# Performance work log

Hardware: AMD Instinct MI355X
Metric: run time of the kernel (lower is better)

## Reference

```python
import jax, jax.numpy as jnp
import numpy as np

N_VOX = 500_000
C = 128
HID = 4 * C
RES = 128  # voxel grid resolution
K_OFFS = 27


def _build_sparse_coords_and_neighbors(seed=0):
    rng = np.random.default_rng(seed)
    lin = rng.choice(RES ** 3, size=N_VOX, replace=False)
    z = lin // (RES * RES)
    y = (lin // RES) % RES
    x = lin % RES
    # padded grid (RES+2)^3 so boundary lookups are in-bounds
    P = RES + 2
    grid = -np.ones(P * P * P, dtype=np.int64)
    z1, y1, x1 = z + 1, y + 1, x + 1
    grid[z1 * P * P + y1 * P + x1] = np.arange(N_VOX)
    offs = np.array([[dz, dy, dx] for dz in (-1, 0, 1) for dy in (-1, 0, 1) for dx in (-1, 0, 1)], dtype=np.int64)  # [27,3]
    nz = z1[:, None] + offs[None, :, 0]
    ny = y1[:, None] + offs[None, :, 1]
    nx = x1[:, None] + offs[None, :, 2]
    nbr = grid[nz * P * P + ny * P + nx]  # [N,27], -1 if neighbor voxel inactive
    return nbr.astype(np.int32)


def setup_inputs() -> dict:
    key = jax.random.key(0)
    ks = jax.random.split(key, 8)
    nbr = _build_sparse_coords_and_neighbors()
    scale = 0.02
    return {
        "feats": jax.random.normal(ks[0], (N_VOX, C), jnp.float32),
        "neighbor_idx": jnp.asarray(nbr),
        "conv_w": jax.random.normal(ks[1], (K_OFFS, C, C), jnp.float32) * scale,
        "conv_b": jax.random.normal(ks[2], (C,), jnp.float32) * scale,
        "ln_g": jnp.ones((C,), jnp.float32),
        "ln_b": jnp.zeros((C,), jnp.float32),
        "w1": jax.random.normal(ks[3], (C, HID), jnp.float32) * scale,
        "b1": jax.random.normal(ks[4], (HID,), jnp.float32) * scale,
        "w2": jax.random.normal(ks[5], (HID, C), jnp.float32) * scale,
        "b2": jax.random.normal(ks[6], (C,), jnp.float32) * scale,
    }


def _forward(feats, neighbor_idx, conv_w, conv_b, ln_g, ln_b, w1, b1, w2, b2):
    n, c = feats.shape
    # submanifold sparse conv3d: pad a zero row for missing (-1) neighbors
    f_pad = jnp.concatenate([feats, jnp.zeros((1, c), feats.dtype)], axis=0)
    idx = jnp.where(neighbor_idx < 0, n, neighbor_idx)  # [N,27]
    h = jnp.broadcast_to(conv_b, (n, c))
    for k in range(K_OFFS):  # fixed small kernel-offset loop; per-offset gather + GEMM
        h = h + f_pad[idx[:, k]] @ conv_w[k]
    # LayerNorm32 (fp32 math), eps=1e-6, affine
    h32 = h.astype(jnp.float32)
    mu = h32.mean(-1, keepdims=True)
    var = h32.var(-1, keepdims=True)
    hn = ((h32 - mu) * jax.lax.rsqrt(var + 1e-6) * ln_g + ln_b).astype(feats.dtype)
    # MLP: Linear -> SiLU -> Linear
    m = jax.nn.silu(hn @ w1 + b1) @ w2 + b2
    # residual h + x on sparse feats
    return m + feats


def reference(feats, neighbor_idx, conv_w, conv_b, ln_g, ln_b, w1, b1, w2, b2):
    return _forward(feats, neighbor_idx, conv_w, conv_b, ln_g, ln_b, w1, b1, w2, b2)
```

## Files before the change

### kernel.cpp

```cpp
#include <hip/hip_runtime.h>
#include <stdint.h>

#define NVOX 500000
#define NPAD 500224
#define ZERO_OFF (NVOX * 128)

typedef float  f32x4  __attribute__((ext_vector_type(4)));
typedef short  short8 __attribute__((ext_vector_type(8)));

__device__ __forceinline__ short f2bf(float x){
  unsigned u = __float_as_uint(x);
  unsigned r = (u + 0x7fffu + ((u >> 16) & 1u)) >> 16;
  return (short)r;
}

__device__ __forceinline__ void gload_lds16(const void* g, void* l){
  __builtin_amdgcn_global_load_lds(
      (const __attribute__((address_space(1))) unsigned int*)(uintptr_t)g,
      (__attribute__((address_space(3))) unsigned int*)(unsigned int)(uintptr_t)l,
      16, 0, 0);
}

__global__ void cast_feats_kernel(const float* __restrict__ f, short* __restrict__ t){
  long i = ((long)blockIdx.x * 256 + threadIdx.x) * 8;
  float4 a = *(const float4*)(f + i);
  float4 b = *(const float4*)(f + i + 4);
  short8 o = { f2bf(a.x), f2bf(a.y), f2bf(a.z), f2bf(a.w),
               f2bf(b.x), f2bf(b.y), f2bf(b.z), f2bf(b.w) };
  *(short8*)(t + i) = o;
}

__global__ void prep_nbr_kernel(const int* __restrict__ nbr, int* __restrict__ nbrT){
  __shared__ int lds_n[6912];
  const int tid = threadIdx.x;
  const long base = (long)blockIdx.x * 6912;
  #pragma unroll
  for (int i = 0; i < 27; i++){
    long g = base + i*256 + tid;
    lds_n[i*256 + tid] = (g < (long)NVOX*27) ? nbr[g] : -1;
  }
  __syncthreads();
  const int row = blockIdx.x * 256 + tid;
  #pragma unroll
  for (int k = 0; k < 27; k++){
    int id = lds_n[tid*27 + k];
    nbrT[(size_t)k*NPAD + row] = (id < 0 ? NVOX : id) * 128;
  }
}

__global__ void prep_weights_kernel(const float* __restrict__ cw, const float* __restrict__ w1,
                                    const float* __restrict__ w2,
                                    short* __restrict__ cw_sw, short* __restrict__ w1_sw,
                                    short* __restrict__ w2_sw){
  int t = blockIdx.x * 256 + threadIdx.x;
  if (t < 55296){
    int k = t >> 11, rem = t & 2047;
    int nf = rem >> 8, ks = (rem >> 6) & 3, l = rem & 63;
    int g = l >> 4, c = l & 15;
    short8 o;
    #pragma unroll
    for (int j = 0; j < 8; j++){
      int kk = ks*32 + g*8 + j;
      o[j] = f2bf(cw[(k*128 + kk)*128 + nf*16 + c]);
    }
    *(short8*)(cw_sw + (size_t)t*8) = o;
  } else if (t < 63488){
    int u = t - 55296;
    int nf = u >> 8, ks = (u >> 6) & 3, l = u & 63;
    int g = l >> 4, c = l & 15;
    short8 o;
    #pragma unroll
    for (int j = 0; j < 8; j++){
      int kk = ks*32 + g*8 + j;
      o[j] = f2bf(w1[kk*512 + nf*16 + c]);
    }
    *(short8*)(w1_sw + (size_t)u*8) = o;
  } else {
    int u = t - 63488;
    int ch = u >> 10, rem = u & 1023;
    int nf = rem >> 7, ks2 = (rem >> 6) & 1, l = u & 63;
    int g = l >> 4, c = l & 15;
    short8 o;
    #pragma unroll
    for (int j = 0; j < 8; j++){
      int k = ch*64 + ks2*32 + g*8 + j;
      o[j] = f2bf(w2[k*128 + nf*16 + c]);
    }
    *(short8*)(w2_sw + (size_t)u*8) = o;
  }
}

__global__ __launch_bounds__(256, 2)
void conv_ln_pf_kernel(const short* __restrict__ table, const int* __restrict__ nbrT,
                       const short* __restrict__ cw_sw,
                       const float* __restrict__ conv_b, const float* __restrict__ ln_g,
                       const float* __restrict__ ln_b, short* __restrict__ hn16){
  __shared__ __align__(16) short lds_b[2][16384];
  const int tid = threadIdx.x;
  const int lane = tid & 63, wv = tid >> 6;
  const int l15 = lane & 15, lg = lane >> 4;
  const int rowbase = blockIdx.x * 256 + wv * 64;
  const int rowi = rowbase + l15;

  f32x4 acc[4][8];
  #pragma unroll
  for (int m = 0; m < 4; m++)
    #pragma unroll
    for (int n = 0; n < 8; n++)
      acc[m][n] = f32x4{0.f, 0.f, 0.f, 0.f};

  int idx_c[4], idx_n[4];
  #pragma unroll
  for (int m = 0; m < 4; m++) idx_c[m] = nbrT[rowi + m*16];
  #pragma unroll
  for (int m = 0; m < 4; m++) idx_n[m] = nbrT[NPAD + rowi + m*16];
  short8 afp[2][4];
  #pragma unroll
  for (int ks = 0; ks < 2; ks++)
    #pragma unroll
    for (int m = 0; m < 4; m++)
      afp[ks][m] = *(const short8*)(table + (size_t)(unsigned)idx_c[m] + ks*32 + lg*8);
  {
    const char* src = (const char*)cw_sw;
    char* dst = (char*)&lds_b[0][0];
    #pragma unroll
    for (int i = 0; i < 8; i++){ int off = i*4096 + tid*16; gload_lds16(src+off, dst+off); }
  }

  for (int k = 0; k < 27; k++){
    const int buf = k & 1;
    __syncthreads();
    short8 af2[4], af3[4];
    #pragma unroll
    for (int m = 0; m < 4; m++)
      af2[m] = *(const short8*)(table + (size_t)(unsigned)idx_c[m] + 64 + lg*8);
    #pragma unroll
    for (int m = 0; m < 4; m++)
      af3[m] = *(const short8*)(table + (size_t)(unsigned)idx_c[m] + 96 + lg*8);
    int idx_n2[4];
    #pragma unroll
    for (int m = 0; m < 4; m++)
      idx_n2[m] = (k + 2 < 27) ? nbrT[(size_t)(k+2)*NPAD + rowi + m*16] : ZERO_OFF;
    if (k + 1 < 27){
      const char* src = (const char*)cw_sw + (size_t)(k+1)*32768;
      char* dst = (char*)&lds_b[buf ^ 1][0];
      #pragma unroll
      for (int i = 0; i < 8; i++){ int off = i*4096 + tid*16; gload_lds16(src+off, dst+off); }
    }

    const short* bbase = &lds_b[buf][0];
    #pragma unroll
    for (int ks = 0; ks < 2; ks++){
      #pragma unroll
      for (int n = 0; n < 8; n++){
        short8 b = *(const short8*)(bbase + ((n*4 + ks)*64 + lane)*8);
        #pragma unroll
        for (int m = 0; m < 4; m++)
          acc[m][n] = __builtin_amdgcn_mfma_f32_16x16x32_bf16(afp[ks][m], b, acc[m][n], 0, 0, 0);
      }
    }
    short8 afp_n[2][4];
    #pragma unroll
    for (int ks = 0; ks < 2; ks++)
      #pragma unroll
      for (int m = 0; m < 4; m++)
        afp_n[ks][m] = *(const short8*)(table + (size_t)(unsigned)idx_n[m] + ks*32 + lg*8);
    #pragma unroll
    for (int n = 0; n < 8; n++){
      short8 b = *(const short8*)(bbase + ((n*4 + 2)*64 + lane)*8);
      #pragma unroll
      for (int m = 0; m < 4; m++)
        acc[m][n] = __builtin_amdgcn_mfma_f32_16x16x32_bf16(af2[m], b, acc[m][n], 0, 0, 0);
    }
    #pragma unroll
    for (int n = 0; n < 8; n++){
      short8 b = *(const short8*)(bbase + ((n*4 + 3)*64 + lane)*8);
      #pragma unroll
      for (int m = 0; m < 4; m++)
        acc[m][n] = __builtin_amdgcn_mfma_f32_16x16x32_bf16(af3[m], b, acc[m][n], 0, 0, 0);
    }
    #pragma unroll
    for (int m = 0; m < 4; m++){
      afp[0][m] = afp_n[0][m];
      afp[1][m] = afp_n[1][m];
      idx_c[m] = idx_n[m];
      idx_n[m] = idx_n2[m];
    }
  }

  float cb[8], g8[8], be[8];
  #pragma unroll
  for (int n = 0; n < 8; n++){
    cb[n] = conv_b[n*16 + l15];
    g8[n] = ln_g[n*16 + l15];
    be[n] = ln_b[n*16 + l15];
  }
  #pragma unroll
  for (int m = 0; m < 4; m++){
    #pragma unroll
    for (int r = 0; r < 4; r++){
      float s = 0.f, s2 = 0.f;
      #pragma unroll
      for (int n = 0; n < 8; n++){
        float h = acc[m][n][r] + cb[n];
        acc[m][n][r] = h;
        s += h; s2 += h*h;
      }
      #pragma unroll
      for (int msk = 1; msk < 16; msk <<= 1){
        s  += __shfl_xor(s,  msk);
        s2 += __shfl_xor(s2, msk);
      }
      float mu  = s  * 0.0078125f;
      float var = s2 * 0.0078125f - mu*mu;
      float rs  = rsqrtf(var + 1e-6f);
      int row = rowbase + m*16 + lg*4 + r;
      if (row < NVOX){
        #pragma unroll
        for (int n = 0; n < 8; n++){
          float hv = (acc[m][n][r] - mu) * rs * g8[n] + be[n];
          hn16[(size_t)row*128 + n*16 + l15] = f2bf(hv);
        }
      }
    }
  }
}

template<bool TBL>
__global__ __launch_bounds__(256, 2)
void conv_ln_kernel(const short* __restrict__ table, const float* __restrict__ feats,
                    const int* __restrict__ nbr, const short* __restrict__ cw_sw,
                    const float* __restrict__ conv_b, const float* __restrict__ ln_g,
                    const float* __restrict__ ln_b, short* __restrict__ hn16){
  __shared__ __align__(16) short lds_b[2][16384];
  const int tid = threadIdx.x;
  const int lane = tid & 63, wv = tid >> 6;
  const int l15 = lane & 15, lg = lane >> 4;
  const int rowbase = blockIdx.x * 256 + wv * 64;

  f32x4 acc[4][8];
  #pragma unroll
  for (int m = 0; m < 4; m++)
    #pragma unroll
    for (int n = 0; n < 8; n++)
      acc[m][n] = f32x4{0.f, 0.f, 0.f, 0.f};

  {
    const char* src = (const char*)cw_sw;
    char* dst = (char*)&lds_b[0][0];
    #pragma unroll
    for (int i = 0; i < 8; i++){ int off = i*4096 + tid*16; gload_lds16(src+off, dst+off); }
  }

  for (int k = 0; k < 27; k++){
    const int buf = k & 1;
    __syncthreads();
    if (k + 1 < 27){
      const char* src = (const char*)cw_sw + (size_t)(k+1)*32768;
      char* dst = (char*)&lds_b[buf ^ 1][0];
      #pragma unroll
      for (int i = 0; i < 8; i++){ int off = i*4096 + tid*16; gload_lds16(src+off, dst+off); }
    }
    int idxr[4];
    #pragma unroll
    for (int m = 0; m < 4; m++){
      int row = rowbase + m*16 + l15;
      row = row < NVOX ? row : NVOX - 1;
      int id = nbr[row*27 + k];
      idxr[m] = TBL ? (id < 0 ? NVOX : id) : id;
    }
    const short* bbase = &lds_b[buf][0];
    #pragma unroll
    for (int ks = 0; ks < 4; ks++){
      short8 af[4];
      #pragma unroll
      for (int m = 0; m < 4; m++){
        if constexpr (TBL){
          af[m] = *(const short8*)(table + (size_t)idxr[m]*128 + ks*32 + lg*8);
        } else {
          if (idxr[m] < 0){
            af[m] = short8{0,0,0,0,0,0,0,0};
          } else {
            const float* p = feats + (size_t)idxr[m]*128 + ks*32 + lg*8;
            float4 x = *(const float4*)p;
            float4 y = *(const float4*)(p + 4);
            af[m] = short8{ f2bf(x.x), f2bf(x.y), f2bf(x.z), f2bf(x.w),
                            f2bf(y.x), f2bf(y.y), f2bf(y.z), f2bf(y.w) };
          }
        }
      }
      #pragma unroll
      for (int n = 0; n < 8; n++){
        short8 b = *(const short8*)(bbase + ((n*4 + ks)*64 + lane)*8);
        #pragma unroll
        for (int m = 0; m < 4; m++)
          acc[m][n] = __builtin_amdgcn_mfma_f32_16x16x32_bf16(af[m], b, acc[m][n], 0, 0, 0);
      }
    }
  }

  float cb[8], g8[8], be[8];
  #pragma unroll
  for (int n = 0; n < 8; n++){
    cb[n] = conv_b[n*16 + l15];
    g8[n] = ln_g[n*16 + l15];
    be[n] = ln_b[n*16 + l15];
  }
  #pragma unroll
  for (int m = 0; m < 4; m++){
    #pragma unroll
    for (int r = 0; r < 4; r++){
      float s = 0.f, s2 = 0.f;
      #pragma unroll
      for (int n = 0; n < 8; n++){
        float h = acc[m][n][r] + cb[n];
        acc[m][n][r] = h;
        s += h; s2 += h*h;
      }
      #pragma unroll
      for (int msk = 1; msk < 16; msk <<= 1){
        s  += __shfl_xor(s,  msk);
        s2 += __shfl_xor(s2, msk);
      }
      float mu  = s  * 0.0078125f;
      float var = s2 * 0.0078125f - mu*mu;
      float rs  = rsqrtf(var + 1e-6f);
      int row = rowbase + m*16 + lg*4 + r;
      if (row < NVOX){
        #pragma unroll
        for (int n = 0; n < 8; n++){
          float hv = (acc[m][n][r] - mu) * rs * g8[n] + be[n];
          hn16[(size_t)row*128 + n*16 + l15] = f2bf(hv);
        }
      }
    }
  }
}

__global__ __launch_bounds__(256, 2)
void mlp_kernel(const short* __restrict__ hn16, const float* __restrict__ feats,
                const short* __restrict__ w1_sw, const short* __restrict__ w2_sw,
                const float* __restrict__ b1, const float* __restrict__ b2,
                float* __restrict__ out){
  __shared__ __align__(16) short lds_w[2][16384];
  __shared__ __align__(16) short lds_act[4*2048];
  const int tid = threadIdx.x;
  const int lane = tid & 63, wv = tid >> 6;
  const int l15 = lane & 15, lg = lane >> 4;
  const int rowbase = blockIdx.x * 128 + wv * 32;
  short* actw = &lds_act[wv * 2048];

  f32x4 acc2[2][8];
  #pragma unroll
  for (int m = 0; m < 2; m++)
    #pragma unroll
    for (int n = 0; n < 8; n++)
      acc2[m][n] = f32x4{0.f, 0.f, 0.f, 0.f};

  int rowg[2];
  #pragma unroll
  for (int m = 0; m < 2; m++){
    int row = rowbase + m*16 + l15;
    rowg[m] = row < NVOX ? row : NVOX - 1;
  }

  short8 a1[4][2];
  #pragma unroll
  for (int ks = 0; ks < 4; ks++)
    #pragma unroll
    for (int m = 0; m < 2; m++)
      a1[ks][m] = *(const short8*)(hn16 + (size_t)rowg[m]*128 + ks*32 + lg*8);

  {
    const char* s1 = (const char*)w1_sw;
    const char* s2 = (const char*)w2_sw;
    char* dst = (char*)&lds_w[0][0];
    #pragma unroll
    for (int i = 0; i < 4; i++){ int off = i*4096 + tid*16; gload_lds16(s1+off, dst+off); }
    #pragma unroll
    for (int i = 0; i < 4; i++){ int off = i*4096 + tid*16; gload_lds16(s2+off, dst+16384+off); }
  }

  for (int ch = 0; ch < 8; ch++){
    const int buf = ch & 1;
    __syncthreads();
    if (ch + 1 < 8){
      const char* s1 = (const char*)w1_sw + (size_t)(ch+1)*16384;
      const char* s2 = (const char*)w2_sw + (size_t)(ch+1)*16384;
      char* dst = (char*)&lds_w[buf ^ 1][0];
      #pragma unroll
      for (int i = 0; i < 4; i++){ int off = i*4096 + tid*16; gload_lds16(s1+off, dst+off); }
      #pragma unroll
      for (int i = 0; i < 4; i++){ int off = i*4096 + tid*16; gload_lds16(s2+off, dst+16384+off); }
    }
    const short* w1c = &lds_w[buf][0];
    const short* w2c = &lds_w[buf][8192];

    #pragma unroll
    for (int n = 0; n < 4; n++){
      f32x4 p0 = f32x4{0.f,0.f,0.f,0.f};
      f32x4 p1 = f32x4{0.f,0.f,0.f,0.f};
      #pragma unroll
      for (int ks = 0; ks < 4; ks++){
        short8 b = *(const short8*)(w1c + ((n*4 + ks)*64 + lane)*8);
        p0 = __builtin_amdgcn_mfma_f32_16x16x32_bf16(a1[ks][0], b, p0, 0, 0, 0);
        p1 = __builtin_amdgcn_mfma_f32_16x16x32_bf16(a1[ks][1], b, p1, 0, 0, 0);
      }
      float bb1 = b1[ch*64 + n*16 + l15];
      #pragma unroll
      for (int r = 0; r < 4; r++){
        float x0 = p0[r] + bb1;
        float x1 = p1[r] + bb1;
        float s0 = x0 / (1.f + __expf(-x0));
        float s1 = x1 / (1.f + __expf(-x1));
        int r0 = lg*4 + r;
        int r1 = 16 + lg*4 + r;
        actw[(r0*64 + n*16 + l15) ^ ((r0 & 7) << 3)] = f2bf(s0);
        actw[(r1*64 + n*16 + l15) ^ ((r1 & 7) << 3)] = f2bf(s1);
      }
    }

    #pragma unroll
    for (int ks2 = 0; ks2 < 2; ks2++){
      short8 a2[2];
      #pragma unroll
      for (int m = 0; m < 2; m++){
        int rowloc = m*16 + l15;
        a2[m] = *(const short8*)(actw + ((rowloc*64 + ks2*32 + lg*8) ^ ((rowloc & 7) << 3)));
      }
      #pragma unroll
      for (int n = 0; n < 8; n++){
        short8 b = *(const short8*)(w2c + ((n*2 + ks2)*64 + lane)*8);
        #pragma unroll
        for (int m = 0; m < 2; m++)
          acc2[m][n] = __builtin_amdgcn_mfma_f32_16x16x32_bf16(a2[m], b, acc2[m][n], 0, 0, 0);
      }
    }
  }

  float bb2[8];
  #pragma unroll
  for (int n = 0; n < 8; n++) bb2[n] = b2[n*16 + l15];
  #pragma unroll
  for (int m = 0; m < 2; m++)
    #pragma unroll
    for (int n = 0; n < 8; n++)
      #pragma unroll
      for (int r = 0; r < 4; r++){
        int row = rowbase + m*16 + lg*4 + r;
        if (row < NVOX){
          size_t ci = (size_t)row*128 + n*16 + l15;
          out[ci] = acc2[m][n][r] + bb2[n] + feats[ci];
        }
      }
}

extern "C" void kernel_launch(void* const* d_in, const int* in_sizes, int n_in,
                              void* d_out, int out_size, void* d_ws, size_t ws_size,
                              hipStream_t stream){
  const float* feats = (const float*)d_in[0];
  const int*   nbr   = (const int*)  d_in[1];
  const float* cw    = (const float*)d_in[2];
  const float* cb    = (const float*)d_in[3];
  const float* lng   = (const float*)d_in[4];
  const float* lnb   = (const float*)d_in[5];
  const float* w1    = (const float*)d_in[6];
  const float* b1    = (const float*)d_in[7];
  const float* w2    = (const float*)d_in[8];
  const float* b2    = (const float*)d_in[9];
  float* out = (float*)d_out;

  char* ws = (char*)d_ws;
  const size_t TABLE_B = (size_t)(NVOX + 1) * 256;
  const size_t HN_B    = (size_t)NVOX * 256;
  const size_t CW_B    = 55296u * 16u;
  const size_t W1_B    = 8192u * 16u;
  const size_t W2_B    = 8192u * 16u;
  const size_t NBRT_B  = (size_t)27 * NPAD * 4;
  const size_t need_full = TABLE_B + HN_B + CW_B + W1_B + W2_B;
  const size_t need_pf   = need_full + NBRT_B;

  if (ws_size >= need_pf){
    short* table = (short*)ws;
    short* hn16  = (short*)(ws + TABLE_B);
    short* cw_sw = (short*)(ws + TABLE_B + HN_B);
    short* w1_sw = (short*)(ws + TABLE_B + HN_B + CW_B);
    short* w2_sw = (short*)(ws + TABLE_B + HN_B + CW_B + W1_B);
    int*   nbrT  = (int*)  (ws + need_full);

    cast_feats_kernel<<<31250, 256, 0, stream>>>(feats, table);
    hipMemsetAsync((void*)(table + (size_t)NVOX * 128), 0, 256, stream);
    prep_nbr_kernel<<<1954, 256, 0, stream>>>(nbr, nbrT);
    prep_weights_kernel<<<280, 256, 0, stream>>>(cw, w1, w2, cw_sw, w1_sw, w2_sw);
    conv_ln_pf_kernel<<<1954, 256, 0, stream>>>(table, nbrT, cw_sw, cb, lng, lnb, hn16);
    mlp_kernel<<<3907, 256, 0, stream>>>(hn16, feats, w1_sw, w2_sw, b1, b2, out);
  } else if (ws_size >= need_full){
    short* table = (short*)ws;
    short* hn16  = (short*)(ws + TABLE_B);
    short* cw_sw = (short*)(ws + TABLE_B + HN_B);
    short* w1_sw = (short*)(ws + TABLE_B + HN_B + CW_B);
    short* w2_sw = (short*)(ws + TABLE_B + HN_B + CW_B + W1_B);

    cast_feats_kernel<<<31250, 256, 0, stream>>>(feats, table);
    hipMemsetAsync((void*)(table + (size_t)NVOX * 128), 0, 256, stream);
    prep_weights_kernel<<<280, 256, 0, stream>>>(cw, w1, w2, cw_sw, w1_sw, w2_sw);
    conv_ln_kernel<true><<<1954, 256, 0, stream>>>(table, feats, nbr, cw_sw, cb, lng, lnb, hn16);
    mlp_kernel<<<3907, 256, 0, stream>>>(hn16, feats, w1_sw, w2_sw, b1, b2, out);
  } else {
    short* hn16  = (short*)ws;
    short* cw_sw = (short*)(ws + HN_B);
    short* w1_sw = (short*)(ws + HN_B + CW_B);
    short* w2_sw = (short*)(ws + HN_B + CW_B + W1_B);

    prep_weights_kernel<<<280, 256, 0, stream>>>(cw, w1, w2, cw_sw, w1_sw, w2_sw);
    conv_ln_kernel<false><<<1954, 256, 0, stream>>>(nullptr, feats, nbr, cw_sw, cb, lng, lnb, hn16);
    mlp_kernel<<<3907, 256, 0, stream>>>(hn16, feats, w1_sw, w2_sw, b1, b2, out);
  }
}
```

Baseline: 929.8 us.

## Halve conv tile and split weight slices into K-halves for higher occupancy

The sparse conv+LayerNorm kernel now processes 32 rows per wave (128 per block) instead of 64, and streams each offset's weights in two 16KB K-halves rather than double-buffering full 32KB slices. This cuts the accumulator registers and LDS per block so four blocks can be resident per CU, which should better hide the latency of the random neighbour gathers. The weight-prep layout is reordered to match, and the fallback kernel's indexing is adjusted. In exchange each weight slice is reused by fewer rows, there are two barriers per offset, and the register prefetch of next-offset activations is dropped.

```diff
diff --git a/kernel.cpp b/kernel.cpp
--- a/kernel.cpp
+++ b/kernel.cpp
@@ -63,7 +63,8 @@
       int kk = ks*32 + g*8 + j;
       o[j] = f2bf(cw[(k*128 + kk)*128 + nf*16 + c]);
     }
-    *(short8*)(cw_sw + (size_t)t*8) = o;
+    size_t dst = (size_t)(k*2 + (ks >> 1))*8192 + (size_t)(nf*2 + (ks & 1))*512 + (size_t)l*8;
+    *(short8*)(cw_sw + dst) = o;
   } else if (t < 63488){
     int u = t - 55296;
     int nf = u >> 8, ks = (u >> 6) & 3, l = u & 63;
@@ -90,102 +91,107 @@
   }
 }
 
-__global__ __launch_bounds__(256, 2)
-void conv_ln_pf_kernel(const short* __restrict__ table, const int* __restrict__ nbrT,
+__global__ __launch_bounds__(256, 4)
+void conv_ln_v4_kernel(const short* __restrict__ table, const int* __restrict__ nbrT,
                        const short* __restrict__ cw_sw,
                        const float* __restrict__ conv_b, const float* __restrict__ ln_g,
                        const float* __restrict__ ln_b, short* __restrict__ hn16){
-  __shared__ __align__(16) short lds_b[2][16384];
+  __shared__ __align__(16) short lds_b[2][8192];
   const int tid = threadIdx.x;
   const int lane = tid & 63, wv = tid >> 6;
   const int l15 = lane & 15, lg = lane >> 4;
-  const int rowbase = blockIdx.x * 256 + wv * 64;
+  const int rowbase = blockIdx.x * 128 + wv * 32;
   const int rowi = rowbase + l15;
 
-  f32x4 acc[4][8];
-  #pragma unroll
-  for (int m = 0; m < 4; m++)
+  f32x4 acc[2][8];
+  #pragma unroll
+  for (int m = 0; m < 2; m++)
     #pragma unroll
     for (int n = 0; n < 8; n++)
       acc[m][n] = f32x4{0.f, 0.f, 0.f, 0.f};
 
-  int idx_c[4], idx_n[4];
-  #pragma unroll
-  for (int m = 0; m < 4; m++) idx_c[m] = nbrT[rowi + m*16];
-  #pragma unroll
-  for (int m = 0; m < 4; m++) idx_n[m] = nbrT[NPAD + rowi + m*16];
-  short8 afp[2][4];
-  #pragma unroll
-  for (int ks = 0; ks < 2; ks++)
-    #pragma unroll
-    for (int m = 0; m < 4; m++)
-      afp[ks][m] = *(const short8*)(table + (size_t)(unsigned)idx_c[m] + ks*32 + lg*8);
+  int idx_c[2], idx_n[2];
+  #pragma unroll
+  for (int m = 0; m < 2; m++) idx_c[m] = nbrT[rowi + m*16];
+  #pragma unroll
+  for (int m = 0; m < 2; m++) idx_n[m] = nbrT[NPAD + rowi + m*16];
+
   {
     const char* src = (const char*)cw_sw;
     char* dst = (char*)&lds_b[0][0];
     #pragma unroll
-    for (int i = 0; i < 8; i++){ int off = i*4096 + tid*16; gload_lds16(src+off, dst+off); }
+    for (int i = 0; i < 4; i++){ int off = i*4096 + tid*16; gload_lds16(src+off, dst+off); }
   }
 
   for (int k = 0; k < 27; k++){
-    const int buf = k & 1;
     __syncthreads();
-    short8 af2[4], af3[4];
-    #pragma unroll
-    for (int m = 0; m < 4; m++)
-      af2[m] = *(const short8*)(table + (size_t)(unsigned)idx_c[m] + 64 + lg*8);
-    #pragma unroll
-    for (int m = 0; m < 4; m++)
-      af3[m] = *(const short8*)(table + (size_t)(unsigned)idx_c[m] + 96 + lg*8);
-    int idx_n2[4];
-    #pragma unroll
-    for (int m = 0; m < 4; m++)
-      idx_n2[m] = (k + 2 < 27) ? nbrT[(size_t)(k+2)*NPAD + rowi + m*16] : ZERO_OFF;
+    {
+      const char* src = (const char*)cw_sw + (size_t)(k*2 + 1)*16384;
+      char* dst = (char*)&lds_b[1][0];
+      #pragma unroll
+      for (int i = 0; i < 4; i++){ int off = i*4096 + tid*16; gload_lds16(src+off, dst+off); }
+    }
+    {
+      short8 af0[2], af1[2];
+      #pragma unroll
+      for (int m = 0; m < 2; m++)
+        af0[m] = *(const short8*)(table + (size_t)(unsigned)idx_c[m] + lg*8);
+      #pragma unroll
+      for (int m = 0; m < 2; m++)
+        af1[m] = *(const short8*)(table + (size_t)(unsigned)idx_c[m] + 32 + lg*8);
+      const short* b0 = &lds_b[0][0];
+      #pragma unroll
+      for (int n = 0; n < 8; n++){
+        short8 b = *(const short8*)(b0 + ((n*2 + 0)*64 + lane)*8);
+        #pragma unroll
+        for (int m = 0; m < 2; m++)
+          acc[m][n] = __builtin_amdgcn_mfma_f32_16x16x32_bf16(af0[m], b, acc[m][n], 0, 0, 0);
+      }
+      #pragma unroll
+      for (int n = 0; n < 8; n++){
+        short8 b = *(const short8*)(b0 + ((n*2 + 1)*64 + lane)*8);
+        #pragma unroll
+        for (int m = 0; m < 2; m++)
+          acc[m][n] = __builtin_amdgcn_mfma_f32_16x16x32_bf16(af1[m], b, acc[m][n], 0, 0, 0);
+      }
+    }
+    __syncthreads();
     if (k + 1 < 27){
       const char* src = (const char*)cw_sw + (size_t)(k+1)*32768;
-      char* dst = (char*)&lds_b[buf ^ 1][0];
-      #pragma unroll
-      for (int i = 0; i < 8; i++){ int off = i*4096 + tid*16; gload_lds16(src+off, dst+off); }
-    }
-
-    const short* bbase = &lds_b[buf][0];
-    #pragma unroll
-    for (int ks = 0; ks < 2; ks++){
-      #pragma unroll
-      for (int n = 0; n < 8; n++){
-        short8 b = *(const short8*)(bbase + ((n*4 + ks)*64 + lane)*8);
-        #pragma unroll
-        for (int m = 0; m < 4; m++)
-          acc[m][n] = __builtin_amdgcn_mfma_f32_16x16x32_bf16(afp[ks][m], b, acc[m][n], 0, 0, 0);
-      }
-    }
-    short8 afp_n[2][4];
-    #pragma unroll
-    for (int ks = 0; ks < 2; ks++)
-      #pragma unroll
-      for (int m = 0; m < 4; m++)
-        afp_n[ks][m] = *(const short8*)(table + (size_t)(unsigned)idx_n[m] + ks*32 + lg*8);
-    #pragma unroll
-    for (int n = 0; n < 8; n++){
-      short8 b = *(const short8*)(bbase + ((n*4 + 2)*64 + lane)*8);
-      #pragma unroll
-      for (int m = 0; m < 4; m++)
-        acc[m][n] = __builtin_amdgcn_mfma_f32_16x16x32_bf16(af2[m], b, acc[m][n], 0, 0, 0);
-    }
-    #pragma unroll
-    for (int n = 0; n < 8; n++){
-      short8 b = *(const short8*)(bbase + ((n*4 + 3)*64 + lane)*8);
-      #pragma unroll
-      for (int m = 0; m < 4; m++)
-        acc[m][n] = __builtin_amdgcn_mfma_f32_16x16x32_bf16(af3[m], b, acc[m][n], 0, 0, 0);
-    }
-    #pragma unroll
-    for (int m = 0; m < 4; m++){
-      afp[0][m] = afp_n[0][m];
-      afp[1][m] = afp_n[1][m];
-      idx_c[m] = idx_n[m];
-      idx_n[m] = idx_n2[m];
-    }
+      char* dst = (char*)&lds_b[0][0];
+      #pragma unroll
+      for (int i = 0; i < 4; i++){ int off = i*4096 + tid*16; gload_lds16(src+off, dst+off); }
+    }
+    int idx_n2[2];
+    #pragma unroll
+    for (int m = 0; m < 2; m++)
+      idx_n2[m] = (k + 2 < 27) ? nbrT[(size_t)(k+2)*NPAD + rowi + m*16] : ZERO_OFF;
+    {
+      short8 af2[2], af3[2];
+      #pragma unroll
+      for (int m = 0; m < 2; m++)
+        af2[m] = *(const short8*)(table + (size_t)(unsigned)idx_c[m] + 64 + lg*8);
+      #pragma unroll
+      for (int m = 0; m < 2; m++)
+        af3[m] = *(const short8*)(table + (size_t)(unsigned)idx_c[m] + 96 + lg*8);
+      const short* b1 = &lds_b[1][0];
+      #pragma unroll
+      for (int n = 0; n < 8; n++){
+        short8 b = *(const short8*)(b1 + ((n*2 + 0)*64 + lane)*8);
+        #pragma unroll
+        for (int m = 0; m < 2; m++)
+          acc[m][n] = __builtin_amdgcn_mfma_f32_16x16x32_bf16(af2[m], b, acc[m][n], 0, 0, 0);
+      }
+      #pragma unroll
+      for (int n = 0; n < 8; n++){
+        short8 b = *(const short8*)(b1 + ((n*2 + 1)*64 + lane)*8);
+        #pragma unroll
+        for (int m = 0; m < 2; m++)
+          acc[m][n] = __builtin_amdgcn_mfma_f32_16x16x32_bf16(af3[m], b, acc[m][n], 0, 0, 0);
+      }
+    }
+    #pragma unroll
+    for (int m = 0; m < 2; m++){ idx_c[m] = idx_n[m]; idx_n[m] = idx_n2[m]; }
   }
 
   float cb[8], g8[8], be[8];
@@ -196,7 +202,7 @@
     be[n] = ln_b[n*16 + l15];
   }
   #pragma unroll
-  for (int m = 0; m < 4; m++){
+  for (int m = 0; m < 2; m++){
     #pragma unroll
     for (int r = 0; r < 4; r++){
       float s = 0.f, s2 = 0.f;
@@ -291,7 +297,7 @@
       }
       #pragma unroll
       for (int n = 0; n < 8; n++){
-        short8 b = *(const short8*)(bbase + ((n*4 + ks)*64 + lane)*8);
+        short8 b = *(const short8*)(bbase + (ks >> 1)*8192 + (((n*2 + (ks & 1))*64) + lane)*8);
         #pragma unroll
         for (int m = 0; m < 4; m++)
           acc[m][n] = __builtin_amdgcn_mfma_f32_16x16x32_bf16(af[m], b, acc[m][n], 0, 0, 0);
@@ -492,7 +498,7 @@
     hipMemsetAsync((void*)(table + (size_t)NVOX * 128), 0, 256, stream);
     prep_nbr_kernel<<<1954, 256, 0, stream>>>(nbr, nbrT);
     prep_weights_kernel<<<280, 256, 0, stream>>>(cw, w1, w2, cw_sw, w1_sw, w2_sw);
-    conv_ln_pf_kernel<<<1954, 256, 0, stream>>>(table, nbrT, cw_sw, cb, lng, lnb, hn16);
+    conv_ln_v4_kernel<<<3907, 256, 0, stream>>>(table, nbrT, cw_sw, cb, lng, lnb, hn16);
     mlp_kernel<<<3907, 256, 0, stream>>>(hn16, feats, w1_sw, w2_sw, b1, b2, out);
   } else if (ws_size >= need_full){
     short* table = (short*)ws;
```

Measured after the change: 912.2 us. About the same (-1.9%).
